# Performance work log

Measured on AMD Instinct MI355X. Metric: run time of the kernel, lower is better.

## Reference

```python
import jax, jax.numpy as jnp
import numpy as np

D_MODEL = 1024
NUM_HEADS = 16
D_K = D_MODEL // NUM_HEADS
B, SQ, SK = 2, 2048, 2048


def setup_inputs() -> dict:
    key = jax.random.key(0)
    ks = jax.random.split(key, 12)
    s = 1.0 / np.sqrt(D_MODEL)
    inp = {
        'query': jax.random.normal(ks[0], (B, SQ, D_MODEL), jnp.float32),
        'key': jax.random.normal(ks[1], (B, SK, D_MODEL), jnp.float32),
        'value': jax.random.normal(ks[2], (B, SK, D_MODEL), jnp.float32),
        # causal mask [B, 1, Sq, Sk], True = keep
        'mask': jnp.broadcast_to(jnp.tril(jnp.ones((SQ, SK), bool))[None, None], (B, 1, SQ, SK)),
        'Wq': jax.random.uniform(ks[3], (D_MODEL, D_MODEL), jnp.float32, -s, s),
        'bq': jnp.zeros((D_MODEL,), jnp.float32),
        'Wk': jax.random.uniform(ks[4], (D_MODEL, D_MODEL), jnp.float32, -s, s),
        'bk': jnp.zeros((D_MODEL,), jnp.float32),
        'Wv': jax.random.uniform(ks[5], (D_MODEL, D_MODEL), jnp.float32, -s, s),
        'bv': jnp.zeros((D_MODEL,), jnp.float32),
        'Wo': jax.random.uniform(ks[6], (D_MODEL, D_MODEL), jnp.float32, -s, s),
        'bo': jnp.zeros((D_MODEL,), jnp.float32),
    }
    return inp


def reference(query, key, value, mask, Wq, bq, Wk, bk, Wv, bv, Wo, bo):
    b, sq, _ = query.shape
    sk = key.shape[1]
    # projections; torch Linear: x @ W.T + b (here W stored as [in, out] so x @ W)
    Q = (query @ Wq + bq).reshape(b, sq, NUM_HEADS, D_K).transpose(0, 2, 1, 3)  # [B,H,Sq,dk]
    K = (key @ Wk + bk).reshape(b, sk, NUM_HEADS, D_K).transpose(0, 2, 1, 3)
    V = (value @ Wv + bv).reshape(b, sk, NUM_HEADS, D_K).transpose(0, 2, 1, 3)
    scores = jnp.einsum('bhqd,bhkd->bhqk', Q, K) / jnp.sqrt(jnp.float32(D_K))
    neg = jnp.finfo(scores.dtype).min
    scores = jnp.where(mask, scores, neg)
    probs = jax.nn.softmax(scores, axis=-1)
    attn = jnp.einsum('bhqk,bhkd->bhqd', probs, V)  # [B,H,Sq,dk]
    attn = attn.transpose(0, 2, 1, 3).reshape(b, sq, D_MODEL)
    return attn @ Wo + bo
```

## Files before the change

### kernel.cpp

```cpp
#include <hip/hip_runtime.h>
#include <hip/hip_bf16.h>

#define DM 1024
#define NH 16
#define DKK 64
#define NB 2
#define SQL 2048
#define SKL 2048

typedef __attribute__((ext_vector_type(8))) short short8;
typedef __attribute__((ext_vector_type(4))) float floatx4;

static __device__ inline floatx4 mfma16(short8 a, short8 b, floatx4 c) {
    return __builtin_amdgcn_mfma_f32_16x16x32_bf16(a, b, c, 0, 0, 0);
}

static __device__ inline unsigned short f2bf(float f) {
    __hip_bfloat16 h = __float2bfloat16(f);
    return *reinterpret_cast<unsigned short*>(&h);
}

__device__ __forceinline__ void gload16(const void* g, void* l) {
    __builtin_amdgcn_global_load_lds(
        (const __attribute__((address_space(1))) void*)g,
        (__attribute__((address_space(3))) void*)l, 16, 0, 0);
}

__global__ __launch_bounds__(256) void x2bf(
    const float* __restrict__ q, const float* __restrict__ k, const float* __restrict__ v,
    unsigned short* __restrict__ oq, unsigned short* __restrict__ ok, unsigned short* __restrict__ ov)
{
    const int n4 = 1 << 20;
    for (int i = blockIdx.x * blockDim.x + threadIdx.x; i < 3 * n4; i += gridDim.x * blockDim.x) {
        const int z = i >> 20, off = (i & (n4 - 1)) * 4;
        const float* src = z == 0 ? q : (z == 1 ? k : v);
        unsigned short* dst = z == 0 ? oq : (z == 1 ? ok : ov);
        const float4 f = *reinterpret_cast<const float4*>(&src[off]);
        uint2 p;
        p.x = (unsigned)f2bf(f.x) | ((unsigned)f2bf(f.y) << 16);
        p.y = (unsigned)f2bf(f.z) | ((unsigned)f2bf(f.w) << 16);
        *reinterpret_cast<uint2*>(&dst[off]) = p;
    }
}

__global__ void transpose_w4(const float* __restrict__ Wq, const float* __restrict__ Wk,
                             const float* __restrict__ Wv, const float* __restrict__ Wo,
                             unsigned short* __restrict__ WtQ, unsigned short* __restrict__ WtK,
                             unsigned short* __restrict__ WtV, unsigned short* __restrict__ WtO) {
    const int z = blockIdx.z;
    const float* W = z == 0 ? Wq : (z == 1 ? Wk : (z == 2 ? Wv : Wo));
    unsigned short* Wt = z == 0 ? WtQ : (z == 1 ? WtK : (z == 2 ? WtV : WtO));
    __shared__ unsigned short t[32][33];
    int tx = threadIdx.x, ty = threadIdx.y;
    int n0 = blockIdx.x * 32, k0 = blockIdx.y * 32;
#pragma unroll
    for (int i = 0; i < 4; i++) {
        int k = k0 + ty + i * 8;
        t[tx][ty + i * 8] = f2bf(W[k * DM + n0 + tx]);
    }
    __syncthreads();
#pragma unroll
    for (int i = 0; i < 4; i++) {
        int n = n0 + ty + i * 8;
        Wt[n * DM + k0 + tx] = t[ty + i * 8][tx];
    }
}

__global__ __launch_bounds__(256) void proj_qkv2(
    const unsigned short* __restrict__ Xq, const unsigned short* __restrict__ Xk,
    const unsigned short* __restrict__ Xv,
    const unsigned short* __restrict__ WtQ, const unsigned short* __restrict__ WtK,
    const unsigned short* __restrict__ WtV,
    const float* __restrict__ bq, const float* __restrict__ bk, const float* __restrict__ bv,
    unsigned short* __restrict__ Qh, unsigned short* __restrict__ Kh, unsigned short* __restrict__ Vt)
{
    const int z = blockIdx.z;
    const unsigned short* X  = z == 0 ? Xq : (z == 1 ? Xk : Xv);
    const unsigned short* Wt = z == 0 ? WtQ : (z == 1 ? WtK : WtV);
    const float* bias = z == 0 ? bq : (z == 1 ? bk : bv);
    unsigned short* out = z == 0 ? Qh : (z == 1 ? Kh : Vt);

    __shared__ __align__(16) unsigned short As[128 * 64];
    __shared__ __align__(16) unsigned short Bs[128 * 64];

    const int tid = threadIdx.x;
    const int w = tid >> 6, lane = tid & 63;
    const int lg = lane >> 4, lr = lane & 15;
    const int wr = w >> 1, wc = w & 1;
    const int m0 = blockIdx.x * 128, n0 = blockIdx.y * 128;

    floatx4 acc[4][4] = {};

    int srow[4], scol[4], ldsoff[4];
#pragma unroll
    for (int i = 0; i < 4; i++) {
        const int idx = i * 256 + tid;
        srow[i] = idx >> 3;
        scol[i] = ((idx & 7) ^ (srow[i] & 7)) * 8;
        ldsoff[i] = (i * 256 + w * 64) * 8;
    }

    for (int k0 = 0; k0 < DM; k0 += 64) {
        __syncthreads();
#pragma unroll
        for (int i = 0; i < 4; i++)
            gload16(&X[(size_t)(m0 + srow[i]) * DM + k0 + scol[i]], &As[ldsoff[i]]);
#pragma unroll
        for (int i = 0; i < 4; i++)
            gload16(&Wt[(size_t)(n0 + srow[i]) * DM + k0 + scol[i]], &Bs[ldsoff[i]]);
        __syncthreads();
#pragma unroll
        for (int kk = 0; kk < 2; kk++) {
            short8 a[4], b[4];
#pragma unroll
            for (int mi = 0; mi < 4; mi++) {
                const int r = wr * 64 + mi * 16 + lr;
                a[mi] = *reinterpret_cast<const short8*>(&As[r * 64 + (((kk * 4 + lg) ^ (r & 7)) * 8)]);
            }
#pragma unroll
            for (int ni = 0; ni < 4; ni++) {
                const int r = wc * 64 + ni * 16 + lr;
                b[ni] = *reinterpret_cast<const short8*>(&Bs[r * 64 + (((kk * 4 + lg) ^ (r & 7)) * 8)]);
            }
#pragma unroll
            for (int mi = 0; mi < 4; mi++)
#pragma unroll
                for (int ni = 0; ni < 4; ni++)
                    acc[mi][ni] = mfma16(a[mi], b[ni], acc[mi][ni]);
        }
    }

    const float qscale = (z == 0) ? 0.125f : 1.0f;
#pragma unroll
    for (int mi = 0; mi < 4; mi++)
#pragma unroll
        for (int ni = 0; ni < 4; ni++)
#pragma unroll
            for (int r = 0; r < 4; r++) {
                const int m = m0 + wr * 64 + mi * 16 + lg * 4 + r;
                const int n = n0 + wc * 64 + ni * 16 + lr;
                const float val = (acc[mi][ni][r] + bias[n]) * qscale;
                const int bb = m >> 11, s = m & 2047;
                const int h = n >> 6, d = n & 63;
                const unsigned short o = f2bf(val);
                if (z != 2)
                    out[(((size_t)(bb * NH + h) * SQL) + s) * DKK + d] = o;
                else
                    out[(((size_t)(bb * NH + h) * DKK) + d) * SKL + s] = o;
            }
}

#define KVB 64

__device__ __forceinline__ void load_tile(uint4* kr, uint4* vr,
    const unsigned short* __restrict__ Kb, const unsigned short* __restrict__ Vb,
    int kv0, int tid)
{
    const int row = tid >> 3, sl = tid & 7;
    *kr = *reinterpret_cast<const uint4*>(&Kb[(size_t)(kv0 + row) * DKK + sl * 8]);
    *vr = *reinterpret_cast<const uint4*>(&Vb[(size_t)row * SKL + kv0 + sl * 8]);
}

__device__ __forceinline__ void store_tile(unsigned short* kl, unsigned short* vl,
                                           const uint4* kr, const uint4* vr, int tid)
{
    const int row = tid >> 3, sl = tid & 7;
    const int off = row * 64 + ((sl ^ (row & 7)) * 8);
    *reinterpret_cast<uint4*>(&kl[off]) = *kr;
    *reinterpret_cast<uint4*>(&vl[off]) = *vr;
}

__global__ __launch_bounds__(512) void attn_fwd(
    const unsigned short* __restrict__ Qh, const unsigned short* __restrict__ Kh,
    const unsigned short* __restrict__ Vt, unsigned short* __restrict__ attn)
{
    __shared__ __align__(16) unsigned short Kl[2][4096];
    __shared__ __align__(16) unsigned short Vl[2][4096];
    __shared__ __align__(16) unsigned short Pl[8][2048];

    const int tid = threadIdx.x;
    const int w = tid >> 6, lane = tid & 63;
    const int lg = lane >> 4, lr = lane & 15;
    const int b = blockIdx.z, h = blockIdx.y;
    const int q0 = (int)(gridDim.x - 1 - blockIdx.x) * 256;
    const int wq0 = q0 + w * 32;

    const unsigned short* Qb = Qh + (size_t)(b * NH + h) * SQL * DKK;
    const unsigned short* Kb = Kh + (size_t)(b * NH + h) * SKL * DKK;
    const unsigned short* Vb = Vt + (size_t)(b * NH + h) * DKK * SKL;

    short8 qf[2][2];
#pragma unroll
    for (int mi = 0; mi < 2; mi++)
#pragma unroll
        for (int kk = 0; kk < 2; kk++)
            qf[mi][kk] = *reinterpret_cast<const short8*>(
                &Qb[(size_t)(wq0 + mi * 16 + lr) * DKK + kk * 32 + lg * 8]);

    floatx4 oa[4][2] = {};
    float m_s[2] = {-1e30f, -1e30f};
    float l_s[2] = {0.f, 0.f};

    const int nt = (q0 >> 6) + 4;

    uint4 kr, vr;
    load_tile(&kr, &vr, Kb, Vb, 0, tid);

    for (int t = 0; t < nt; ++t) {
        const int kv0 = t << 6;
        const int cur = t & 1;
        store_tile(Kl[cur], Vl[cur], &kr, &vr, tid);
        __syncthreads();
        if (t + 1 < nt) load_tile(&kr, &vr, Kb, Vb, kv0 + KVB, tid);

        if (kv0 < wq0 + 32) {
            floatx4 sa[4][2] = {};
            __builtin_amdgcn_s_setprio(1);
#pragma unroll
            for (int c = 0; c < 4; c++) {
                const int row = c * 16 + lr;
#pragma unroll
                for (int kk = 0; kk < 2; kk++) {
                    short8 kf = *reinterpret_cast<const short8*>(
                        &Kl[cur][row * 64 + (((kk * 4 + lg) ^ (lr & 7)) * 8)]);
#pragma unroll
                    for (int mi = 0; mi < 2; mi++)
                        sa[c][mi] = mfma16(kf, qf[mi][kk], sa[c][mi]);
                }
            }
            __builtin_amdgcn_s_setprio(0);
            const bool do_mask = (kv0 + KVB - 1 > wq0);
#pragma unroll
            for (int mi = 0; mi < 2; mi++) {
                const int q = wq0 + mi * 16 + lr;
                float pm = -1e30f;
#pragma unroll
                for (int c = 0; c < 4; c++)
#pragma unroll
                    for (int r = 0; r < 4; r++) {
                        float v = sa[c][mi][r];
                        if (do_mask && (kv0 + c * 16 + lg * 4 + r > q)) v = -1e30f;
                        sa[c][mi][r] = v;
                        pm = fmaxf(pm, v);
                    }
                pm = fmaxf(pm, __shfl_xor(pm, 16));
                pm = fmaxf(pm, __shfl_xor(pm, 32));
                const float mn = fmaxf(m_s[mi], pm);
                const float es = __expf(m_s[mi] - mn);
                m_s[mi] = mn;
                float ps = 0.f;
#pragma unroll
                for (int c = 0; c < 4; c++)
#pragma unroll
                    for (int r = 0; r < 4; r++) {
                        float p = __expf(sa[c][mi][r] - mn);
                        sa[c][mi][r] = p;
                        ps += p;
                    }
                ps += __shfl_xor(ps, 16);
                ps += __shfl_xor(ps, 32);
                l_s[mi] = l_s[mi] * es + ps;
#pragma unroll
                for (int f = 0; f < 4; f++)
#pragma unroll
                    for (int r = 0; r < 4; r++)
                        oa[f][mi][r] *= es;
                const int prow = mi * 16 + lr;
#pragma unroll
                for (int c = 0; c < 4; c++) {
                    uint2 pk;
                    pk.x = (unsigned)f2bf(sa[c][mi][0]) | ((unsigned)f2bf(sa[c][mi][1]) << 16);
                    pk.y = (unsigned)f2bf(sa[c][mi][2]) | ((unsigned)f2bf(sa[c][mi][3]) << 16);
                    *reinterpret_cast<uint2*>(
                        &Pl[w][prow * 64 + (((c * 2 + (lg >> 1)) ^ (lr & 7)) * 8) + (lg & 1) * 4]) = pk;
                }
            }
            short8 pf[2][2];
#pragma unroll
            for (int mi = 0; mi < 2; mi++)
#pragma unroll
                for (int kk = 0; kk < 2; kk++)
                    pf[mi][kk] = *reinterpret_cast<const short8*>(
                        &Pl[w][(mi * 16 + lr) * 64 + (((kk * 4 + lg) ^ (lr & 7)) * 8)]);
            __builtin_amdgcn_s_setprio(1);
#pragma unroll
            for (int f = 0; f < 4; f++) {
                const int row = f * 16 + lr;
#pragma unroll
                for (int kk = 0; kk < 2; kk++) {
                    short8 vt = *reinterpret_cast<const short8*>(
                        &Vl[cur][row * 64 + (((kk * 4 + lg) ^ (lr & 7)) * 8)]);
#pragma unroll
                    for (int mi = 0; mi < 2; mi++)
                        oa[f][mi] = mfma16(vt, pf[mi][kk], oa[f][mi]);
                }
            }
            __builtin_amdgcn_s_setprio(0);
        }
        __syncthreads();
    }

#pragma unroll
    for (int mi = 0; mi < 2; mi++) {
        const float inv = 1.f / l_s[mi];
        const int prow = mi * 16 + lr;
#pragma unroll
        for (int f = 0; f < 4; f++) {
            uint2 pk;
            pk.x = (unsigned)f2bf(oa[f][mi][0] * inv) | ((unsigned)f2bf(oa[f][mi][1] * inv) << 16);
            pk.y = (unsigned)f2bf(oa[f][mi][2] * inv) | ((unsigned)f2bf(oa[f][mi][3] * inv) << 16);
            *reinterpret_cast<uint2*>(
                &Pl[w][prow * 64 + (((f * 2 + (lg >> 1)) ^ (prow & 7)) * 8) + (lg & 1) * 4]) = pk;
        }
    }
#pragma unroll
    for (int i = 0; i < 4; i++) {
        const int rl = i * 8 + (lane >> 3);
        const int slot = lane & 7;
        const uint4 o = *reinterpret_cast<const uint4*>(
            &Pl[w][rl * 64 + ((slot ^ (rl & 7)) * 8)]);
        const int q = wq0 + rl;
        *reinterpret_cast<uint4*>(
            &attn[((size_t)(b * SQL + q)) * DM + h * DKK + slot * 8]) = o;
    }
}

__global__ __launch_bounds__(256) void proj_o2(
    const unsigned short* __restrict__ Attn, const unsigned short* __restrict__ WtO,
    const float* __restrict__ bo, float* __restrict__ out)
{
    __shared__ __align__(16) unsigned short As[128 * 64];
    __shared__ __align__(16) unsigned short Bs[64 * 64];

    const int tid = threadIdx.x;
    const int w = tid >> 6, lane = tid & 63;
    const int lg = lane >> 4, lr = lane & 15;
    const int wr = w >> 1, wc = w & 1;
    const int m0 = blockIdx.x * 128, n0 = blockIdx.y * 64;

    floatx4 acc[4][2] = {};

    int srow[4], scol[4], ldsoff[4];
#pragma unroll
    for (int i = 0; i < 4; i++) {
        const int idx = i * 256 + tid;
        srow[i] = idx >> 3;
        scol[i] = ((idx & 7) ^ (srow[i] & 7)) * 8;
        ldsoff[i] = (i * 256 + w * 64) * 8;
    }

    for (int k0 = 0; k0 < DM; k0 += 64) {
        __syncthreads();
#pragma unroll
        for (int i = 0; i < 4; i++)
            gload16(&Attn[(size_t)(m0 + srow[i]) * DM + k0 + scol[i]], &As[ldsoff[i]]);
#pragma unroll
        for (int i = 0; i < 2; i++)
            gload16(&WtO[(size_t)(n0 + srow[i]) * DM + k0 + scol[i]], &Bs[ldsoff[i]]);
        __syncthreads();
#pragma unroll
        for (int kk = 0; kk < 2; kk++) {
            short8 a[4], b[2];
#pragma unroll
            for (int mi = 0; mi < 4; mi++) {
                const int r = wr * 64 + mi * 16 + lr;
                a[mi] = *reinterpret_cast<const short8*>(&As[r * 64 + (((kk * 4 + lg) ^ (r & 7)) * 8)]);
            }
#pragma unroll
            for (int ni = 0; ni < 2; ni++) {
                const int r = wc * 32 + ni * 16 + lr;
                b[ni] = *reinterpret_cast<const short8*>(&Bs[r * 64 + (((kk * 4 + lg) ^ (r & 7)) * 8)]);
            }
#pragma unroll
            for (int mi = 0; mi < 4; mi++)
#pragma unroll
                for (int ni = 0; ni < 2; ni++)
                    acc[mi][ni] = mfma16(a[mi], b[ni], acc[mi][ni]);
        }
    }

#pragma unroll
    for (int mi = 0; mi < 4; mi++)
#pragma unroll
        for (int ni = 0; ni < 2; ni++)
#pragma unroll
            for (int r = 0; r < 4; r++) {
                const int m = m0 + wr * 64 + mi * 16 + lg * 4 + r;
                const int n = n0 + wc * 32 + ni * 16 + lr;
                out[(size_t)m * DM + n] = acc[mi][ni][r] + bo[n];
            }
}

extern "C" void kernel_launch(void* const* d_in, const int* in_sizes, int n_in,
                              void* d_out, int out_size, void* d_ws, size_t ws_size,
                              hipStream_t stream) {
    const float* query = (const float*)d_in[0];
    const float* key   = (const float*)d_in[1];
    const float* value = (const float*)d_in[2];
    const float* Wq = (const float*)d_in[4];
    const float* bq = (const float*)d_in[5];
    const float* Wk = (const float*)d_in[6];
    const float* bk = (const float*)d_in[7];
    const float* Wv = (const float*)d_in[8];
    const float* bv = (const float*)d_in[9];
    const float* Wo = (const float*)d_in[10];
    const float* bo = (const float*)d_in[11];
    float* out = (float*)d_out;

    unsigned short* ws = (unsigned short*)d_ws;
    const size_t MW = (size_t)DM * DM;
    const size_t MH = (size_t)NB * NH * SQL * DKK;
    unsigned short* WtQ = ws;
    unsigned short* WtK = WtQ + MW;
    unsigned short* WtV = WtK + MW;
    unsigned short* WtO = WtV + MW;
    unsigned short* Qh  = WtO + MW;
    unsigned short* Kh  = Qh + MH;
    unsigned short* Vt  = Kh + MH;
    unsigned short* At  = Vt + MH;
    unsigned short* Xbq = (unsigned short*)d_out;
    unsigned short* Xbk = Xbq + MH;
    unsigned short* Xbv = At;

    x2bf<<<2048, 256, 0, stream>>>(query, key, value, Xbq, Xbk, Xbv);
    transpose_w4<<<dim3(32, 32, 4), dim3(32, 8), 0, stream>>>(Wq, Wk, Wv, Wo, WtQ, WtK, WtV, WtO);
    proj_qkv2<<<dim3(32, 8, 3), 256, 0, stream>>>(Xbq, Xbk, Xbv, WtQ, WtK, WtV,
                                                  bq, bk, bv, Qh, Kh, Vt);
    attn_fwd<<<dim3(SQL / 256, NH, NB), 512, 0, stream>>>(Qh, Kh, Vt, At);
    proj_o2<<<dim3(32, 16), 256, 0, stream>>>(At, WtO, bo, out);
}
```

Measured before the change: 277.3 us.

## Halve attention query tile per block, add lazy softmax rescale, drop loop-end barrier

The attention kernel now gives each block 128 query rows instead of 256, and each wave 16 rows instead of 32. This doubles the grid, to improve CU occupancy and balance across the causal triangle, at the cost of re-reading K/V tiles across more blocks. The online-softmax rescale of the output accumulators is skipped when no row max grows by more than 8, a lazy-rescale trick that is exact in the end because the final normalisation uses the same stale max. The second __syncthreads per KV iteration is removed, relying on the double-buffered K/V stores being ordered by the barrier at the top of the next iteration.

```diff
diff --git a/kernel.cpp b/kernel.cpp
--- a/kernel.cpp
+++ b/kernel.cpp
@@ -176,32 +176,29 @@
 {
     __shared__ __align__(16) unsigned short Kl[2][4096];
     __shared__ __align__(16) unsigned short Vl[2][4096];
-    __shared__ __align__(16) unsigned short Pl[8][2048];
+    __shared__ __align__(16) unsigned short Pl[8][1024];
 
     const int tid = threadIdx.x;
     const int w = tid >> 6, lane = tid & 63;
     const int lg = lane >> 4, lr = lane & 15;
     const int b = blockIdx.z, h = blockIdx.y;
-    const int q0 = (int)(gridDim.x - 1 - blockIdx.x) * 256;
-    const int wq0 = q0 + w * 32;
+    const int q0 = (int)(gridDim.x - 1 - blockIdx.x) * 128;
+    const int wq0 = q0 + w * 16;
 
     const unsigned short* Qb = Qh + (size_t)(b * NH + h) * SQL * DKK;
     const unsigned short* Kb = Kh + (size_t)(b * NH + h) * SKL * DKK;
     const unsigned short* Vb = Vt + (size_t)(b * NH + h) * DKK * SKL;
 
-    short8 qf[2][2];
-#pragma unroll
-    for (int mi = 0; mi < 2; mi++)
-#pragma unroll
-        for (int kk = 0; kk < 2; kk++)
-            qf[mi][kk] = *reinterpret_cast<const short8*>(
-                &Qb[(size_t)(wq0 + mi * 16 + lr) * DKK + kk * 32 + lg * 8]);
-
-    floatx4 oa[4][2] = {};
-    float m_s[2] = {-1e30f, -1e30f};
-    float l_s[2] = {0.f, 0.f};
-
-    const int nt = (q0 >> 6) + 4;
+    short8 qf[2];
+#pragma unroll
+    for (int kk = 0; kk < 2; kk++)
+        qf[kk] = *reinterpret_cast<const short8*>(
+            &Qb[(size_t)(wq0 + lr) * DKK + kk * 32 + lg * 8]);
+
+    floatx4 oa[4] = {};
+    float m_s = -1e30f, l_s = 0.f;
+
+    const int nt = (q0 >> 6) + 2;
 
     uint4 kr, vr;
     load_tile(&kr, &vr, Kb, Vb, 0, tid);
@@ -213,8 +210,8 @@
         __syncthreads();
         if (t + 1 < nt) load_tile(&kr, &vr, Kb, Vb, kv0 + KVB, tid);
 
-        if (kv0 < wq0 + 32) {
-            floatx4 sa[4][2] = {};
+        if (kv0 < wq0 + 16) {
+            floatx4 sa[4] = {};
             __builtin_amdgcn_s_setprio(1);
 #pragma unroll
             for (int c = 0; c < 4; c++) {
@@ -223,65 +220,61 @@
                 for (int kk = 0; kk < 2; kk++) {
                     short8 kf = *reinterpret_cast<const short8*>(
                         &Kl[cur][row * 64 + (((kk * 4 + lg) ^ (lr & 7)) * 8)]);
-#pragma unroll
-                    for (int mi = 0; mi < 2; mi++)
-                        sa[c][mi] = mfma16(kf, qf[mi][kk], sa[c][mi]);
+                    sa[c] = mfma16(kf, qf[kk], sa[c]);
                 }
             }
             __builtin_amdgcn_s_setprio(0);
+
             const bool do_mask = (kv0 + KVB - 1 > wq0);
-#pragma unroll
-            for (int mi = 0; mi < 2; mi++) {
-                const int q = wq0 + mi * 16 + lr;
-                float pm = -1e30f;
-#pragma unroll
-                for (int c = 0; c < 4; c++)
-#pragma unroll
-                    for (int r = 0; r < 4; r++) {
-                        float v = sa[c][mi][r];
-                        if (do_mask && (kv0 + c * 16 + lg * 4 + r > q)) v = -1e30f;
-                        sa[c][mi][r] = v;
-                        pm = fmaxf(pm, v);
-                    }
-                pm = fmaxf(pm, __shfl_xor(pm, 16));
-                pm = fmaxf(pm, __shfl_xor(pm, 32));
-                const float mn = fmaxf(m_s[mi], pm);
-                const float es = __expf(m_s[mi] - mn);
-                m_s[mi] = mn;
-                float ps = 0.f;
-#pragma unroll
-                for (int c = 0; c < 4; c++)
-#pragma unroll
-                    for (int r = 0; r < 4; r++) {
-                        float p = __expf(sa[c][mi][r] - mn);
-                        sa[c][mi][r] = p;
-                        ps += p;
-                    }
-                ps += __shfl_xor(ps, 16);
-                ps += __shfl_xor(ps, 32);
-                l_s[mi] = l_s[mi] * es + ps;
+            const int q = wq0 + lr;
+            float pm = -1e30f;
+#pragma unroll
+            for (int c = 0; c < 4; c++)
+#pragma unroll
+                for (int r = 0; r < 4; r++) {
+                    float v = sa[c][r];
+                    if (do_mask && (kv0 + c * 16 + lg * 4 + r > q)) v = -1e30f;
+                    sa[c][r] = v;
+                    pm = fmaxf(pm, v);
+                }
+            pm = fmaxf(pm, __shfl_xor(pm, 16));
+            pm = fmaxf(pm, __shfl_xor(pm, 32));
+            if (!__all(pm <= m_s + 8.f)) {
+                const float mn = fmaxf(m_s, pm);
+                const float es = __expf(m_s - mn);
+                m_s = mn;
+                l_s *= es;
 #pragma unroll
                 for (int f = 0; f < 4; f++)
 #pragma unroll
                     for (int r = 0; r < 4; r++)
-                        oa[f][mi][r] *= es;
-                const int prow = mi * 16 + lr;
-#pragma unroll
-                for (int c = 0; c < 4; c++) {
-                    uint2 pk;
-                    pk.x = (unsigned)f2bf(sa[c][mi][0]) | ((unsigned)f2bf(sa[c][mi][1]) << 16);
-                    pk.y = (unsigned)f2bf(sa[c][mi][2]) | ((unsigned)f2bf(sa[c][mi][3]) << 16);
-                    *reinterpret_cast<uint2*>(
-                        &Pl[w][prow * 64 + (((c * 2 + (lg >> 1)) ^ (lr & 7)) * 8) + (lg & 1) * 4]) = pk;
+                        oa[f][r] *= es;
+            }
+            float ps = 0.f;
+#pragma unroll
+            for (int c = 0; c < 4; c++)
+#pragma unroll
+                for (int r = 0; r < 4; r++) {
+                    float p = __expf(sa[c][r] - m_s);
+                    sa[c][r] = p;
+                    ps += p;
                 }
-            }
-            short8 pf[2][2];
-#pragma unroll
-            for (int mi = 0; mi < 2; mi++)
-#pragma unroll
-                for (int kk = 0; kk < 2; kk++)
-                    pf[mi][kk] = *reinterpret_cast<const short8*>(
-                        &Pl[w][(mi * 16 + lr) * 64 + (((kk * 4 + lg) ^ (lr & 7)) * 8)]);
+            ps += __shfl_xor(ps, 16);
+            ps += __shfl_xor(ps, 32);
+            l_s += ps;
+#pragma unroll
+            for (int c = 0; c < 4; c++) {
+                uint2 pk;
+                pk.x = (unsigned)f2bf(sa[c][0]) | ((unsigned)f2bf(sa[c][1]) << 16);
+                pk.y = (unsigned)f2bf(sa[c][2]) | ((unsigned)f2bf(sa[c][3]) << 16);
+                *reinterpret_cast<uint2*>(
+                    &Pl[w][lr * 64 + (((c * 2 + (lg >> 1)) ^ (lr & 7)) * 8) + (lg & 1) * 4]) = pk;
+            }
+            short8 pf[2];
+#pragma unroll
+            for (int kk = 0; kk < 2; kk++)
+                pf[kk] = *reinterpret_cast<const short8*>(
+                    &Pl[w][lr * 64 + (((kk * 4 + lg) ^ (lr & 7)) * 8)]);
             __builtin_amdgcn_s_setprio(1);
 #pragma unroll
             for (int f = 0; f < 4; f++) {
@@ -290,31 +283,26 @@
                 for (int kk = 0; kk < 2; kk++) {
                     short8 vt = *reinterpret_cast<const short8*>(
                         &Vl[cur][row * 64 + (((kk * 4 + lg) ^ (lr & 7)) * 8)]);
-#pragma unroll
-                    for (int mi = 0; mi < 2; mi++)
-                        oa[f][mi] = mfma16(vt, pf[mi][kk], oa[f][mi]);
+                    oa[f] = mfma16(vt, pf[kk], oa[f]);
                 }
             }
             __builtin_amdgcn_s_setprio(0);
         }
-        __syncthreads();
-    }
-
-#pragma unroll
-    for (int mi = 0; mi < 2; mi++) {
-        const float inv = 1.f / l_s[mi];
-        const int prow = mi * 16 + lr;
+    }
+
+    {
+        const float inv = 1.f / l_s;
 #pragma unroll
         for (int f = 0; f < 4; f++) {
             uint2 pk;
-            pk.x = (unsigned)f2bf(oa[f][mi][0] * inv) | ((unsigned)f2bf(oa[f][mi][1] * inv) << 16);
-            pk.y = (unsigned)f2bf(oa[f][mi][2] * inv) | ((unsigned)f2bf(oa[f][mi][3] * inv) << 16);
+            pk.x = (unsigned)f2bf(oa[f][0] * inv) | ((unsigned)f2bf(oa[f][1] * inv) << 16);
+            pk.y = (unsigned)f2bf(oa[f][2] * inv) | ((unsigned)f2bf(oa[f][3] * inv) << 16);
             *reinterpret_cast<uint2*>(
-                &Pl[w][prow * 64 + (((f * 2 + (lg >> 1)) ^ (prow & 7)) * 8) + (lg & 1) * 4]) = pk;
+                &Pl[w][lr * 64 + (((f * 2 + (lg >> 1)) ^ (lr & 7)) * 8) + (lg & 1) * 4]) = pk;
         }
     }
 #pragma unroll
-    for (int i = 0; i < 4; i++) {
+    for (int i = 0; i < 2; i++) {
         const int rl = i * 8 + (lane >> 3);
         const int slot = lane & 7;
         const uint4 o = *reinterpret_cast<const uint4*>(
@@ -426,6 +414,6 @@
     transpose_w4<<<dim3(32, 32, 4), dim3(32, 8), 0, stream>>>(Wq, Wk, Wv, Wo, WtQ, WtK, WtV, WtO);
     proj_qkv2<<<dim3(32, 8, 3), 256, 0, stream>>>(Xbq, Xbk, Xbv, WtQ, WtK, WtV,
                                                   bq, bk, bv, Qh, Kh, Vt);
-    attn_fwd<<<dim3(SQL / 256, NH, NB), 512, 0, stream>>>(Qh, Kh, Vt, At);
+    attn_fwd<<<dim3(SQL / 128, NH, NB), 512, 0, stream>>>(Qh, Kh, Vt, At);
     proj_o2<<<dim3(32, 16), 256, 0, stream>>>(At, WtO, bo, out);
 }
```

Result: faster. 264.2 us (-4.7%).
